# Kernel optimization log

Hardware: AMD Instinct MI355X
Metric: run time of the kernel (lower is better)

Reference implementation:

```python
import jax, jax.numpy as jnp
import numpy as np

B, CIN, COUT, H, W, K = 32, 256, 256, 64, 64, 3


def setup_inputs() -> dict:
    key = jax.random.key(0)
    k1, k2, k3 = jax.random.split(key, 3)
    x = jax.random.normal(k1, (B, CIN, H, W), dtype=jnp.float32)
    # kaiming_uniform_ with a=sqrt(5): bound = sqrt(6 / ((1 + a^2) * fan_in)) = sqrt(1/fan_in)
    fan_in = CIN * K * K
    bound = float(np.sqrt(1.0 / fan_in))
    weight = jax.random.uniform(k2, (COUT, CIN, K, K), dtype=jnp.float32,
                                minval=-bound, maxval=bound)
    bias = jax.random.normal(k3, (COUT,), dtype=jnp.float32)
    return {"x": x, "weight": weight, "bias": bias}


def reference(x, weight, bias):
    # CustomConvnd with kernel=3, stride=1, padding=1 (module doubles it, pad
    # helper splits around center -> 1 element each side, zero padding),
    # equivalent to a standard 2D cross-correlation like torch Conv2d.
    out = jax.lax.conv_general_dilated(
        x, weight,
        window_strides=(1, 1),
        padding=((1, 1), (1, 1)),
        dimension_numbers=("NCHW", "OIHW", "NCHW"),
    )
    return out + bias[None, :, None, None]
```

## Files before the change

### kernel.cpp

```cpp
#include <hip/hip_runtime.h>
#include <hip/hip_bf16.h>

typedef __attribute__((ext_vector_type(8))) short short8;
typedef __attribute__((ext_vector_type(16))) float floatx16;

#define BDIM 512

constexpr int kCIN = 256, kCOUT = 256, kH = 64, kW = 64;
constexpr int BK = 32;
constexpr int NCHUNK = kCIN / BK;
constexpr int ROWS = 4;
constexpr int XR = ROWS + 2, XC = 66, NPIX = XR * XC;
constexpr int HW = kH * kW;
constexpr int NSTEP = NCHUNK * 9;

constexpr int XS_PLANE = NPIX * 16;
constexpr int WS_PLANE = 256 * 16;
constexpr int WS_BUF   = 4 * WS_PLANE;

__device__ __forceinline__ unsigned short f2bf(float f) {
    unsigned u = __float_as_uint(f);
    u += 0x7fffu + ((u >> 16) & 1u);
    return (unsigned short)(u >> 16);
}

__global__ void wt_transform_kernel(const float* __restrict__ wsrc,
                                    unsigned short* __restrict__ wt2) {
    int idx = blockIdx.x * 256 + threadIdx.x;
    if (idx >= 9 * 256 * 256) return;
    int j  = idx & 7;
    int co = (idx >> 3) & 255;
    int g  = (idx >> 11) & 3;
    int chunk = (idx >> 13) & 7;
    int kk = idx >> 16;
    int ci = chunk * 32 + g * 8 + j;
    wt2[idx] = f2bf(wsrc[(co * 256 + ci) * 9 + kk]);
}

__global__ __launch_bounds__(BDIM, 2)
void conv3x3_mfma_kernel(const float* __restrict__ x,
                         const unsigned short* __restrict__ wt2,
                         const float* __restrict__ bias,
                         float* __restrict__ out) {
    __shared__ __align__(16) char xs[4 * XS_PLANE];
    __shared__ __align__(16) char ws[2 * WS_BUF];

    const int bid = blockIdx.x;
    const int b  = bid >> 4;
    const int h0 = (bid & 15) * ROWS;

    const int tid = threadIdx.x;
    const int wv  = tid >> 6;
    const int l   = tid & 63;
    const int l31 = l & 31;
    const int hi2 = l >> 5;
    const int cog  = (wv & 1) * 128;
    const int wrow = wv >> 1;

    const float* xb = x + (size_t)b * kCIN * HW;

    floatx16 acc[4][2] = {};

    auto stageW = [&](int st, int chunk, int kk) {
        char* wbuf = ws + (st & 1) * WS_BUF;
        const unsigned short* wp = wt2 + (size_t)(kk * 8 + chunk) * 8192;
        #pragma unroll
        for (int it = 0; it < 2; ++it) {
            int c = wv * 2 + it;
            int g = c >> 2;
            int row0 = (c & 3) * 64;
            const unsigned short* src = wp + (g * 256 + row0 + l) * 8;
            __builtin_amdgcn_global_load_lds(
                (const __attribute__((address_space(1))) unsigned int*)src,
                (__attribute__((address_space(3))) unsigned int*)
                    (wbuf + g * WS_PLANE + row0 * 16),
                16, 0, 0);
        }
    };

    auto stageX = [&](int chunk) {
        const int ci0 = chunk * BK;
        for (int t = tid; t < NPIX * 4; t += BDIM) {
            int g = t / NPIX;
            int rem = t - g * NPIX;
            int r = rem / XC;
            int c = rem - r * XC;
            int ih = h0 - 1 + r;
            int iw = c - 1;
            float v[8];
            if ((unsigned)ih < (unsigned)kH && (unsigned)iw < (unsigned)kW) {
                const float* p = xb + (size_t)(ci0 + g * 8) * HW + ih * kW + iw;
                #pragma unroll
                for (int j = 0; j < 8; ++j) v[j] = p[(size_t)j * HW];
            } else {
                #pragma unroll
                for (int j = 0; j < 8; ++j) v[j] = 0.f;
            }
            union { short8 s8; unsigned short u[8]; } pk;
            #pragma unroll
            for (int j = 0; j < 8; ++j) pk.u[j] = f2bf(v[j]);
            int pix = r * XC + c;
            *(short8*)(xs + g * XS_PLANE + pix * 16) = pk.s8;
        }
    };

    stageX(0);
    stageW(0, 0, 0);
    __syncthreads();

    int chunk = 0, kk = 0;
    for (int st = 0; st < NSTEP; ++st) {
        int kk1 = kk + 1, chunk1 = chunk;
        if (kk1 == 9) { kk1 = 0; chunk1++; }
        if (st < NSTEP - 1) stageW(st + 1, chunk1, kk1);

        const char* wbuf = ws + (st & 1) * WS_BUF;
        const int kh = kk / 3, kwo = kk - kh * 3;
        const int r = wrow + kh;

        short8 a[2][4], bfr[2][2];
        #pragma unroll
        for (int s = 0; s < 2; ++s) {
            const int g = s * 2 + hi2;
            #pragma unroll
            for (int i = 0; i < 4; ++i) {
                int co = cog + i * 32 + l31;
                a[s][i] = *(const short8*)(wbuf + g * WS_PLANE + co * 16);
            }
            #pragma unroll
            for (int f = 0; f < 2; ++f) {
                int pix = r * XC + f * 32 + l31 + kwo;
                bfr[s][f] = *(const short8*)(xs + g * XS_PLANE + pix * 16);
            }
        }
        #pragma unroll
        for (int s = 0; s < 2; ++s)
            #pragma unroll
            for (int i = 0; i < 4; ++i)
                #pragma unroll
                for (int f = 0; f < 2; ++f)
                    acc[i][f] = __builtin_amdgcn_mfma_f32_32x32x16_bf16(
                        a[s][i], bfr[s][f], acc[i][f], 0, 0, 0);
        __syncthreads();

        if (kk == 8 && st < NSTEP - 1) {
            stageX(chunk1);
            __syncthreads();
        }
        kk = kk1; chunk = chunk1;
    }

    float* op = out + (size_t)b * kCOUT * HW + (size_t)(h0 + wrow) * kW;
    #pragma unroll
    for (int i = 0; i < 4; ++i) {
        #pragma unroll
        for (int rg = 0; rg < 16; ++rg) {
            int co = cog + i * 32 + (rg & 3) + 8 * (rg >> 2) + 4 * hi2;
            float bv = bias[co];
            #pragma unroll
            for (int f = 0; f < 2; ++f) {
                op[(size_t)co * HW + f * 32 + l31] = acc[i][f][rg] + bv;
            }
        }
    }
}

extern "C" void kernel_launch(void* const* d_in, const int* in_sizes, int n_in,
                              void* d_out, int out_size, void* d_ws, size_t ws_size,
                              hipStream_t stream) {
    const float* x    = (const float*)d_in[0];
    const float* wsrc = (const float*)d_in[1];
    const float* bias = (const float*)d_in[2];
    float* out = (float*)d_out;
    unsigned short* wt2 = (unsigned short*)d_ws;

    hipLaunchKernelGGL(wt_transform_kernel, dim3((9 * 256 * 256 + 255) / 256),
                       dim3(256), 0, stream, wsrc, wt2);

    hipLaunchKernelGGL(conv3x3_mfma_kernel, dim3(32 * (kH / ROWS)), dim3(BDIM),
                       0, stream, x, wt2, bias, out);
}
```

Baseline: 192.5 us.

## Triple-buffer weights and double-buffer activations with single barrier per step

Weights are prefetched two steps ahead into a three-slot LDS ring, and the input tile is double-buffered so the next channel chunk is staged right after the MFMAs instead of behind an extra barrier. Each step now uses one explicit s_waitcnt (vmcnt(2)) plus a raw s_barrier instead of __syncthreads. This is meant to hide global-load latency and remove the synchronisation stall at chunk boundaries. LDS use rises to about 75 KB per block, which could limit blocks per CU. The hand-set vmcnt count also relies on the exact number of outstanding loads.

```diff
diff --git a/kernel.cpp b/kernel.cpp
--- a/kernel.cpp
+++ b/kernel.cpp
@@ -15,6 +15,7 @@
 constexpr int NSTEP = NCHUNK * 9;
 
 constexpr int XS_PLANE = NPIX * 16;
+constexpr int XS_BUF   = 4 * XS_PLANE;
 constexpr int WS_PLANE = 256 * 16;
 constexpr int WS_BUF   = 4 * WS_PLANE;
 
@@ -42,8 +43,8 @@
                          const unsigned short* __restrict__ wt2,
                          const float* __restrict__ bias,
                          float* __restrict__ out) {
-    __shared__ __align__(16) char xs[4 * XS_PLANE];
-    __shared__ __align__(16) char ws[2 * WS_BUF];
+    __shared__ __align__(16) char xs[2 * XS_BUF];
+    __shared__ __align__(16) char ws[3 * WS_BUF];
 
     const int bid = blockIdx.x;
     const int b  = bid >> 4;
@@ -61,8 +62,9 @@
 
     floatx16 acc[4][2] = {};
 
-    auto stageW = [&](int st, int chunk, int kk) {
-        char* wbuf = ws + (st & 1) * WS_BUF;
+    auto stageW = [&](int st) {
+        int chunk = st / 9, kk = st - chunk * 9;
+        char* wbuf = ws + (st % 3) * WS_BUF;
         const unsigned short* wp = wt2 + (size_t)(kk * 8 + chunk) * 8192;
         #pragma unroll
         for (int it = 0; it < 2; ++it) {
@@ -79,6 +81,7 @@
     };
 
     auto stageX = [&](int chunk) {
+        char* xbuf = xs + (chunk & 1) * XS_BUF;
         const int ci0 = chunk * BK;
         for (int t = tid; t < NPIX * 4; t += BDIM) {
             int g = t / NPIX;
@@ -100,21 +103,22 @@
             #pragma unroll
             for (int j = 0; j < 8; ++j) pk.u[j] = f2bf(v[j]);
             int pix = r * XC + c;
-            *(short8*)(xs + g * XS_PLANE + pix * 16) = pk.s8;
+            *(short8*)(xbuf + g * XS_PLANE + pix * 16) = pk.s8;
         }
     };
 
     stageX(0);
-    stageW(0, 0, 0);
+    stageW(0);
+    stageW(1);
     __syncthreads();
 
     int chunk = 0, kk = 0;
-    for (int st = 0; st < NSTEP; ++st) {
-        int kk1 = kk + 1, chunk1 = chunk;
-        if (kk1 == 9) { kk1 = 0; chunk1++; }
-        if (st < NSTEP - 1) stageW(st + 1, chunk1, kk1);
+    #pragma unroll 1
+    for (int t = 0; t < NSTEP; ++t) {
+        if (t + 2 < NSTEP) stageW(t + 2);
 
-        const char* wbuf = ws + (st & 1) * WS_BUF;
+        const char* wbuf = ws + (t % 3) * WS_BUF;
+        const char* xbuf = xs + (chunk & 1) * XS_BUF;
         const int kh = kk / 3, kwo = kk - kh * 3;
         const int r = wrow + kh;
 
@@ -130,7 +134,7 @@
             #pragma unroll
             for (int f = 0; f < 2; ++f) {
                 int pix = r * XC + f * 32 + l31 + kwo;
-                bfr[s][f] = *(const short8*)(xs + g * XS_PLANE + pix * 16);
+                bfr[s][f] = *(const short8*)(xbuf + g * XS_PLANE + pix * 16);
             }
         }
         #pragma unroll
@@ -141,13 +145,23 @@
                 for (int f = 0; f < 2; ++f)
                     acc[i][f] = __builtin_amdgcn_mfma_f32_32x32x16_bf16(
                         a[s][i], bfr[s][f], acc[i][f], 0, 0, 0);
-        __syncthreads();
 
-        if (kk == 8 && st < NSTEP - 1) {
-            stageX(chunk1);
-            __syncthreads();
+        if (kk == 8 && t < NSTEP - 1) stageX(chunk + 1);
+
+        __builtin_amdgcn_sched_barrier(0);
+        if (t + 2 < NSTEP) {
+            asm volatile("s_waitcnt vmcnt(2) lgkmcnt(0)" ::: "memory");
+        } else if (t + 1 < NSTEP) {
+            asm volatile("s_waitcnt vmcnt(0) lgkmcnt(0)" ::: "memory");
         }
-        kk = kk1; chunk = chunk1;
+        if (t < NSTEP - 1) {
+            __builtin_amdgcn_sched_barrier(0);
+            __builtin_amdgcn_s_barrier();
+            __builtin_amdgcn_sched_barrier(0);
+        }
+
+        kk++;
+        if (kk == 9) { kk = 0; chunk++; }
     }
 
     float* op = out + (size_t)b * kCOUT * HW + (size_t)(h0 + wrow) * kW;
```

Result: slower. 199.3 us (+3.5%).
